# Optimization experiments

Hardware: AMD Instinct MI355X
Metric: run time of the kernel (lower is better)

The kernel has to match this reference:

```python
import jax, jax.numpy as jnp
import numpy as np

B, M, D, H = 2, 2048, 1024, 16
DH = D // H            # 64 head dim
FF = 2624              # GeGLU intermediate size
EPS = 1e-5
ROPE_BASE = 10000.0


def _layernorm(x, g, b):
    mu = jnp.mean(x, axis=-1, keepdims=True)
    var = jnp.mean(jnp.square(x - mu), axis=-1, keepdims=True)
    return (x - mu) * jax.lax.rsqrt(var + EPS) * g + b


def _rope_cos_sin(m, dh):
    # HF-style: inv_freq over even dims; only first dh/2 entries are used by apply_rope
    inv_freq = 1.0 / (ROPE_BASE ** (jnp.arange(0, dh, 2, dtype=jnp.float32) / dh))  # [dh/2]
    ang = jnp.arange(m, dtype=jnp.float32)[:, None] * inv_freq[None, :]             # [M, dh/2]
    return jnp.cos(ang), jnp.sin(ang)


def _apply_rope(x, c, s):
    # x: [B,H,M,dh]; c,s: [M,dh/2] broadcast over B,H. Half-split (non-interleaved) rotation.
    x1, x2 = jnp.split(x, 2, axis=-1)
    return jnp.concatenate([x1 * c - x2 * s, x1 * s + x2 * c], axis=-1)


def setup_inputs() -> dict:
    key = jax.random.key(0)
    ks = jax.random.split(key, 6)
    w = lambda k, shape: (jax.random.normal(k, shape, jnp.float32) * 0.02)
    return {
        "hidden_states": jax.random.normal(ks[0], (B, M, D), jnp.float32),
        "attention_mask": jnp.ones((B, M), jnp.int32),
        "ln1_g": jnp.ones((D,), jnp.float32),
        "ln1_b": jnp.zeros((D,), jnp.float32),
        "Wqkv_w": w(ks[1], (3 * D, D)),
        "Wqkv_b": jnp.zeros((3 * D,), jnp.float32),
        "Wo_w": w(ks[2], (D, D)),
        "ln2_g": jnp.ones((D,), jnp.float32),
        "ln2_b": jnp.zeros((D,), jnp.float32),
        "Wi_w": w(ks[3], (2 * FF, D)),
        "Wmlp_o_w": w(ks[4], (D, FF)),
    }


def reference(hidden_states, attention_mask, ln1_g, ln1_b, Wqkv_w, Wqkv_b, Wo_w,
              ln2_g, ln2_b, Wi_w, Wmlp_o_w):
    x = hidden_states                                    # [B,M,D]
    xn = _layernorm(x, ln1_g, ln1_b)
    qkv = xn @ Wqkv_w.T + Wqkv_b                         # [B,M,3D]
    qkv = qkv.reshape(B, M, 3, H, DH).transpose(0, 3, 1, 2, 4)  # [B,H,M,3,dh]
    q, k, v = qkv[..., 0, :], qkv[..., 1, :], qkv[..., 2, :]    # each [B,H,M,dh]

    c, s = _rope_cos_sin(M, DH)                          # [M, dh/2]
    q = _apply_rope(q, c, s)
    k = _apply_rope(k, c, s)

    scale = 1.0 / np.sqrt(DH)
    scores = jnp.einsum("bhmd,bhnd->bhmn", q, k) * scale  # [B,H,M,M]
    keep = (attention_mask > 0)[:, None, None, :]         # [B,1,1,M] padding mask on keys
    scores = jnp.where(keep, scores, -jnp.inf)
    p = jax.nn.softmax(scores, axis=-1)
    o = jnp.einsum("bhmn,bhnd->bhmd", p, v)               # [B,H,M,dh]

    attn_out = o.transpose(0, 2, 1, 3).reshape(B, M, D)
    x = x + attn_out @ Wo_w.T

    # ModernBERT GeGLU MLP: input, gate = Wi(x).chunk(2); Wo(gelu(input) * gate)
    xn2 = _layernorm(x, ln2_g, ln2_b)
    hg = xn2 @ Wi_w.T                                     # [B,M,2*FF]
    h_in, h_gate = jnp.split(hg, 2, axis=-1)
    x = x + (jax.nn.gelu(h_in) * h_gate) @ Wmlp_o_w.T
    return x
```

## Files before the change

### kernel.cpp

```cpp
#include <hip/hip_runtime.h>
#include <cstdint>
#include <cstddef>

using u16 = unsigned short;
using u32 = uint32_t;

typedef __attribute__((ext_vector_type(8))) short short8;
typedef __attribute__((ext_vector_type(4))) float floatx4;
typedef __attribute__((ext_vector_type(4))) unsigned int uintx4;

#define DEVFN static __device__ __forceinline__

#define QSCALE 0.18033688011112042f

DEVFN u16 f2bf(float f) {
  u32 u = __float_as_uint(f);
  return (u16)((u + 0x7fffu + ((u >> 16) & 1u)) >> 16);
}

DEVFN float b2f(u16 u) { return __uint_as_float(((u32)u) << 16); }

DEVFN u32 pkbf(float lo, float hi) {
  return __builtin_amdgcn_perm(__float_as_uint(hi) + 0x8000u,
                               __float_as_uint(lo) + 0x8000u, 0x07060302u);
}

DEVFN void async_load16(const void* g, const void* lds) {
  __builtin_amdgcn_global_load_lds(
      (const __attribute__((address_space(1))) u32*)(uintptr_t)g,
      (__attribute__((address_space(3))) u32*)(u32)(uintptr_t)lds,
      16, 0, 0);
}

DEVFN void cvt4(const float* __restrict__ src, u16* __restrict__ dst, int i) {
  const float4 v = ((const float4*)src)[i];
  ushort4 o;
  o.x = f2bf(v.x); o.y = f2bf(v.y); o.z = f2bf(v.z); o.w = f2bf(v.w);
  ((ushort4*)dst)[i] = o;
}

__global__ __launch_bounds__(256)
void prep_k(const float* __restrict__ Wqkv, const float* __restrict__ Wo,
            const float* __restrict__ Wi, const float* __restrict__ Wmlp,
            const float* __restrict__ hidden, const float* __restrict__ ln1g,
            const float* __restrict__ ln1b,
            u16* __restrict__ wqkv_bf, u16* __restrict__ wo_bf,
            u16* __restrict__ wi_bf, u16* __restrict__ wmlp_bf,
            float* __restrict__ ct, float* __restrict__ st, u16* __restrict__ xn) {
  const int bid = blockIdx.x;
  const int tid = threadIdx.x;
  __shared__ float red[8];
  if (bid < 256) {
    const int i = bid * 256 + tid;
    const int m = i >> 5, f = i & 31;
    const float inv = exp2f((float)f * -0.41524101186092025f);
    const float ang = (float)m * inv;
    ct[i] = cosf(ang);
    st[i] = sinf(ang);
  } else if (bid < 3328) {
    cvt4(Wqkv, wqkv_bf, (bid - 256) * 256 + tid);
  } else if (bid < 4352) {
    cvt4(Wo, wo_bf, (bid - 3328) * 256 + tid);
  } else if (bid < 9600) {
    const int i = (bid - 4352) * 256 + tid;
    const int i4 = i * 4;
    const int p = i4 >> 10, kc = i4 & 1023;
    const int g = p >> 5, c = p & 31;
    const int srow = (c < 16) ? (g * 16 + c) : (2624 + g * 16 + (c - 16));
    const float4 v = *(const float4*)(Wi + (size_t)srow * 1024 + kc);
    ushort4 o;
    o.x = f2bf(v.x); o.y = f2bf(v.y); o.z = f2bf(v.z); o.w = f2bf(v.w);
    ((ushort4*)wi_bf)[i] = o;
  } else if (bid < 12224) {
    cvt4(Wmlp, wmlp_bf, (bid - 9600) * 256 + tid);
  } else {
    const int row = bid - 12224;
    const float4 v = ((const float4*)(hidden + (size_t)row * 1024))[tid];
    float s = v.x + v.y + v.z + v.w;
    float ss = v.x * v.x + v.y * v.y + v.z * v.z + v.w * v.w;
#pragma unroll
    for (int d = 32; d > 0; d >>= 1) {
      s += __shfl_xor(s, d);
      ss += __shfl_xor(ss, d);
    }
    const int wave = tid >> 6;
    if ((tid & 63) == 0) { red[wave] = s; red[4 + wave] = ss; }
    __syncthreads();
    s = red[0] + red[1] + red[2] + red[3];
    ss = red[4] + red[5] + red[6] + red[7];
    const float mu = s * (1.f / 1024.f);
    const float var = ss * (1.f / 1024.f) - mu * mu;
    const float rr = rsqrtf(var + 1e-5f);
    const float4 gv = ((const float4*)ln1g)[tid];
    const float4 bv = ((const float4*)ln1b)[tid];
    u16* orow = xn + (size_t)row * 1024 + tid * 4;
    orow[0] = f2bf((v.x - mu) * rr * gv.x + bv.x);
    orow[1] = f2bf((v.y - mu) * rr * gv.y + bv.y);
    orow[2] = f2bf((v.z - mu) * rr * gv.z + bv.z);
    orow[3] = f2bf((v.w - mu) * rr * gv.w + bv.w);
  }
}

__global__ __launch_bounds__(256)
void red_ln_k(const float* __restrict__ resid, const u16* __restrict__ p0,
              const u16* __restrict__ p1, const u16* __restrict__ p2,
              const float* __restrict__ g, const float* __restrict__ bb,
              float* __restrict__ outx, u16* __restrict__ outn) {
  const int row = blockIdx.x;
  const int tid = threadIdx.x;
  const size_t base = (size_t)row * 1024;
  const float4 h = ((const float4*)(resid + base))[tid];
  const ushort4 a = ((const ushort4*)(p0 + base))[tid];
  const ushort4 c = ((const ushort4*)(p1 + base))[tid];
  const ushort4 d = ((const ushort4*)(p2 + base))[tid];
  float4 v;
  v.x = h.x + b2f(a.x) + b2f(c.x) + b2f(d.x);
  v.y = h.y + b2f(a.y) + b2f(c.y) + b2f(d.y);
  v.z = h.z + b2f(a.z) + b2f(c.z) + b2f(d.z);
  v.w = h.w + b2f(a.w) + b2f(c.w) + b2f(d.w);
  float s = v.x + v.y + v.z + v.w;
  float ss = v.x * v.x + v.y * v.y + v.z * v.z + v.w * v.w;
#pragma unroll
  for (int dd = 32; dd > 0; dd >>= 1) {
    s += __shfl_xor(s, dd);
    ss += __shfl_xor(ss, dd);
  }
  __shared__ float red[8];
  const int wave = tid >> 6;
  if ((tid & 63) == 0) { red[wave] = s; red[4 + wave] = ss; }
  __syncthreads();
  s = red[0] + red[1] + red[2] + red[3];
  ss = red[4] + red[5] + red[6] + red[7];
  const float mu = s * (1.f / 1024.f);
  const float var = ss * (1.f / 1024.f) - mu * mu;
  const float rr = rsqrtf(var + 1e-5f);
  ((float4*)(outx + base))[tid] = v;
  const float4 gv = ((const float4*)g)[tid];
  const float4 bv = ((const float4*)bb)[tid];
  u16* orow = outn + base + tid * 4;
  orow[0] = f2bf((v.x - mu) * rr * gv.x + bv.x);
  orow[1] = f2bf((v.y - mu) * rr * gv.y + bv.y);
  orow[2] = f2bf((v.z - mu) * rr * gv.z + bv.z);
  orow[3] = f2bf((v.w - mu) * rr * gv.w + bv.w);
}

__global__ void red_add_k(float* __restrict__ out, const u16* __restrict__ p0,
                          const u16* __restrict__ p1, const u16* __restrict__ p2,
                          const u16* __restrict__ p3) {
  const int i = blockIdx.x * 256 + threadIdx.x;
  float4 v = ((const float4*)out)[i];
  const ushort4 a = ((const ushort4*)p0)[i];
  const ushort4 c = ((const ushort4*)p1)[i];
  const ushort4 d = ((const ushort4*)p2)[i];
  const ushort4 e = ((const ushort4*)p3)[i];
  v.x += b2f(a.x) + b2f(c.x) + b2f(d.x) + b2f(e.x);
  v.y += b2f(a.y) + b2f(c.y) + b2f(d.y) + b2f(e.y);
  v.z += b2f(a.z) + b2f(c.z) + b2f(d.z) + b2f(e.z);
  v.w += b2f(a.w) + b2f(c.w) + b2f(d.w) + b2f(e.w);
  ((float4*)out)[i] = v;
}

__global__ __launch_bounds__(256)
void red_att_k(u16* __restrict__ att, const u16* __restrict__ p0,
               const float* __restrict__ li0, const float* __restrict__ li1) {
  const int i = blockIdx.x * 256 + threadIdx.x;
  const int i4 = i * 4;
  const int row = i4 >> 10;
  const int col = i4 & 1023;
  const int b = row >> 11, m = row & 2047;
  const int h = col >> 6;
  const int bhm = (b * 16 + h) * 2048 + m;
  const float rl = 1.f / (li0[bhm] + li1[bhm]);
  const ushort4 a = ((const ushort4*)p0)[i];
  const ushort4 c = ((const ushort4*)att)[i];
  ushort4 o;
  o.x = f2bf((b2f(a.x) + b2f(c.x)) * rl);
  o.y = f2bf((b2f(a.y) + b2f(c.y)) * rl);
  o.z = f2bf((b2f(a.z) + b2f(c.z)) * rl);
  o.w = f2bf((b2f(a.w) + b2f(c.w)) * rl);
  ((ushort4*)att)[i] = o;
}

DEVFN void swizzle_tile(int NT, int& tn, int& tm) {
  const int tpx = gridDim.x >> 3;
  const int p = blockIdx.x;
  const int lid = (p & 7) * tpx + (p >> 3);
  const int band = lid / (8 * NT);
  const int rem = lid - band * 8 * NT;
  tn = (rem >> 3) * 128;
  tm = (band * 8 + (rem & 7)) * 128;
}

struct EpiArgs {
  const float* bias;
  u16* q; u16* kk; u16* vt;
  u16* outbf;
  const float* ct; const float* st;
};

template <int EPI>
__global__ __launch_bounds__(256, 3)
void gemm_k(const u16* __restrict__ A, const u16* __restrict__ B, int K, int NT,
            EpiArgs ea) {
  __shared__ __align__(16) u16 sA[2][4096];
  __shared__ __align__(16) u16 sB[2][4096];
  int tn, tm;
  swizzle_tile(NT, tn, tm);
  const int tid = threadIdx.x;
  const int wave = tid >> 6, lane = tid & 63;
  const int quad = lane >> 4, l15 = lane & 15;
  const int wm = (wave >> 1) * 64, wn = (wave & 1) * 64;

  floatx4 acc[4][4];
#pragma unroll
  for (int i = 0; i < 4; ++i)
#pragma unroll
    for (int j = 0; j < 4; ++j) acc[i][j] = (floatx4){0.f, 0.f, 0.f, 0.f};

  const int srow = lane >> 2;
  const int skc = (lane & 3) * 8;
  const int q0i = wave * 2;
  const int row0 = q0i * 16 + srow;
  const int row1 = row0 + 16;
  const size_t aoff0 = (size_t)(tm + row0) * K + skc;
  const size_t aoff1 = (size_t)(tm + row1) * K + skc;
  const size_t boff0 = (size_t)(tn + row0) * K + skc;
  const size_t boff1 = (size_t)(tn + row1) * K + skc;

  async_load16(A + aoff0, (const char*)sA[0] + q0i * 1024);
  async_load16(B + boff0, (const char*)sB[0] + q0i * 1024);
  async_load16(A + aoff1, (const char*)sA[0] + (q0i + 1) * 1024);
  async_load16(B + boff1, (const char*)sB[0] + (q0i + 1) * 1024);

  int buf = 0;
  for (int k0 = 0; k0 < K; k0 += 32) {
    __syncthreads();
    if (k0 + 32 < K) {
      const int kn = k0 + 32;
      async_load16(A + aoff0 + kn, (const char*)sA[buf ^ 1] + q0i * 1024);
      async_load16(B + boff0 + kn, (const char*)sB[buf ^ 1] + q0i * 1024);
      async_load16(A + aoff1 + kn, (const char*)sA[buf ^ 1] + (q0i + 1) * 1024);
      async_load16(B + boff1 + kn, (const char*)sB[buf ^ 1] + (q0i + 1) * 1024);
    }
    const u16* sAr = sA[buf] + (wm + l15) * 32 + quad * 8;
    const u16* sBr = sB[buf] + (wn + l15) * 32 + quad * 8;
    short8 af[4], bfr[4];
#pragma unroll
    for (int t = 0; t < 4; ++t) af[t] = *(const short8*)(sAr + t * 512);
#pragma unroll
    for (int t = 0; t < 4; ++t) bfr[t] = *(const short8*)(sBr + t * 512);
#pragma unroll
    for (int ti = 0; ti < 4; ++ti)
#pragma unroll
      for (int tj = 0; tj < 4; ++tj)
        acc[ti][tj] = __builtin_amdgcn_mfma_f32_16x16x32_bf16(af[ti], bfr[tj], acc[ti][tj], 0, 0, 0);
    buf ^= 1;
  }

  if constexpr (EPI == 0) {
    const int col0 = tn + wn;
    const int t = col0 >> 10;
    const int h = (col0 & 1023) >> 6;
    if (t == 2) {
#pragma unroll
      for (int ti = 0; ti < 4; ++ti)
#pragma unroll
        for (int r = 0; r < 4; ++r) {
          const int row = tm + wm + ti * 16 + quad * 4 + r;
          const int b = row >> 11, m = row & 2047;
          const int mp = (m & ~31) | ((m & 12) << 1) | ((m & 16) >> 2) | (m & 3);
#pragma unroll
          for (int tj = 0; tj < 4; ++tj) {
            const int dh = tj * 16 + l15;
            const float v = acc[ti][tj][r] + ea.bias[col0 + dh];
            ea.vt[((size_t)((b * 16 + h) * 64 + dh)) * 2048 + mp] = f2bf(v);
          }
        }
    } else {
      u16* dst = (t == 0) ? ea.q : ea.kk;
      const float qs = (t == 0) ? QSCALE : 1.f;
#pragma unroll
      for (int ti = 0; ti < 4; ++ti)
#pragma unroll
        for (int r = 0; r < 4; ++r) {
          const int row = tm + wm + ti * 16 + quad * 4 + r;
          const int b = row >> 11, m = row & 2047;
          u16* drow = dst + ((size_t)(b * 16 + h) * 2048 + m) * 64;
#pragma unroll
          for (int tj = 0; tj < 2; ++tj) {
            const int i = tj * 16 + l15;
            const float x1 = acc[ti][tj][r] + ea.bias[col0 + i];
            const float x2 = acc[ti][tj + 2][r] + ea.bias[col0 + 32 + i];
            const float cs = ea.ct[m * 32 + i];
            const float sn = ea.st[m * 32 + i];
            drow[i] = f2bf((x1 * cs - x2 * sn) * qs);
            drow[32 + i] = f2bf((x1 * sn + x2 * cs) * qs);
          }
        }
    }
  } else {
#pragma unroll
    for (int ti = 0; ti < 4; ++ti)
#pragma unroll
      for (int r = 0; r < 4; ++r) {
        const int row = tm + wm + ti * 16 + quad * 4 + r;
#pragma unroll
        for (int u = 0; u < 2; ++u) {
          const float hin = acc[ti][2 * u][r];
          const float hg = acc[ti][2 * u + 1][r];
          const int a = (((tn + wn) >> 5) + u) * 16 + l15;
          const float t2 = hin + 0.044715f * hin * hin * hin;
          const float e = __builtin_amdgcn_exp2f(t2 * -2.302114768f);
          const float gl = hin * __builtin_amdgcn_rcpf(1.f + e);
          ea.outbf[(size_t)row * 2624 + a] = f2bf(gl * hg);
        }
      }
  }
}

__global__ __launch_bounds__(256, 3)
void gemm_sk4(const u16* __restrict__ A, const u16* __restrict__ B, int K, int NT,
              int kps1, int zsw, int kps2,
              u16* __restrict__ p0, u16* __restrict__ p1,
              u16* __restrict__ p2, u16* __restrict__ p3) {
  __shared__ __align__(16) u16 sA[2][4096];
  __shared__ __align__(16) u16 sB[2][4096];
  int tn, tm;
  swizzle_tile(NT, tn, tm);
  const int z = blockIdx.y;
  int kofs, kps;
  if (z < zsw) { kofs = z * kps1; kps = kps1; }
  else { kofs = zsw * kps1 + (z - zsw) * kps2; kps = kps2; }
  const int tid = threadIdx.x;
  const int wave = tid >> 6, lane = tid & 63;
  const int quad = lane >> 4, l15 = lane & 15;
  const int wm = (wave >> 1) * 64, wn = (wave & 1) * 64;

  floatx4 acc[4][4];
#pragma unroll
  for (int i = 0; i < 4; ++i)
#pragma unroll
    for (int j = 0; j < 4; ++j) acc[i][j] = (floatx4){0.f, 0.f, 0.f, 0.f};

  const int srow = lane >> 2;
  const int skc = (lane & 3) * 8;
  const int q0i = wave * 2;
  const int row0 = q0i * 16 + srow;
  const int row1 = row0 + 16;
  const size_t aoff0 = (size_t)(tm + row0) * K + kofs + skc;
  const size_t aoff1 = (size_t)(tm + row1) * K + kofs + skc;
  const size_t boff0 = (size_t)(tn + row0) * K + kofs + skc;
  const size_t boff1 = (size_t)(tn + row1) * K + kofs + skc;

  async_load16(A + aoff0, (const char*)sA[0] + q0i * 1024);
  async_load16(B + boff0, (const char*)sB[0] + q0i * 1024);
  async_load16(A + aoff1, (const char*)sA[0] + (q0i + 1) * 1024);
  async_load16(B + boff1, (const char*)sB[0] + (q0i + 1) * 1024);

  int buf = 0;
  for (int k0 = 0; k0 < kps; k0 += 32) {
    __syncthreads();
    if (k0 + 32 < kps) {
      const int kn = k0 + 32;
      async_load16(A + aoff0 + kn, (const char*)sA[buf ^ 1] + q0i * 1024);
      async_load16(B + boff0 + kn, (const char*)sB[buf ^ 1] + q0i * 1024);
      async_load16(A + aoff1 + kn, (const char*)sA[buf ^ 1] + (q0i + 1) * 1024);
      async_load16(B + boff1 + kn, (const char*)sB[buf ^ 1] + (q0i + 1) * 1024);
    }
    const u16* sAr = sA[buf] + (wm + l15) * 32 + quad * 8;
    const u16* sBr = sB[buf] + (wn + l15) * 32 + quad * 8;
    short8 af[4], bfr[4];
#pragma unroll
    for (int t = 0; t < 4; ++t) af[t] = *(const short8*)(sAr + t * 512);
#pragma unroll
    for (int t = 0; t < 4; ++t) bfr[t] = *(const short8*)(sBr + t * 512);
#pragma unroll
    for (int ti = 0; ti < 4; ++ti)
#pragma unroll
      for (int tj = 0; tj < 4; ++tj)
        acc[ti][tj] = __builtin_amdgcn_mfma_f32_16x16x32_bf16(af[ti], bfr[tj], acc[ti][tj], 0, 0, 0);
    buf ^= 1;
  }

  u16* part = (z == 0) ? p0 : (z == 1) ? p1 : (z == 2) ? p2 : p3;
#pragma unroll
  for (int ti = 0; ti < 4; ++ti)
#pragma unroll
    for (int r = 0; r < 4; ++r) {
      const int row = tm + wm + ti * 16 + quad * 4 + r;
#pragma unroll
      for (int tj = 0; tj < 4; ++tj)
        part[(size_t)row * 1024 + tn + wn + tj * 16 + l15] = f2bf(acc[ti][tj][r]);
    }
}

DEVFN void attn_stage64(const u16* __restrict__ kg, const u16* __restrict__ vtg,
                        size_t bhk, size_t bhv, int key0, int wave, int lane,
                        const u16* sK, const u16* sV) {
#pragma unroll
  for (int j = 0; j < 4; ++j) {
    const int qi = wave * 4 + j;
    if (qi < 8) {
      async_load16(kg + bhk + (size_t)(key0 + lane) * 64 + qi * 8,
                   (const char*)sK + qi * 1024);
    } else {
      const int vi = qi - 8;
      const int c = vi >> 2, kc = vi & 3;
      async_load16(vtg + bhv + (size_t)lane * 2048 + key0 + c * 32 + kc * 8,
                   (const char*)sV + vi * 1024);
    }
  }
}

__global__ __launch_bounds__(256, 3)
void attn_k(const u16* __restrict__ qg, const u16* __restrict__ kg,
            const u16* __restrict__ vtg, const int* __restrict__ mask,
            u16* __restrict__ p0g, u16* __restrict__ p1g,
            float* __restrict__ li0, float* __restrict__ li1) {
  __shared__ __align__(16) u16 sKV[2][8192];
  const int L = blockIdx.x;
  const int xcd = L & 7, idx = L >> 3;
  const int bh = (xcd << 2) | (idx >> 5);
  const int local = idx & 31;
  const int q0 = (local >> 1) * 128;
  const int z = local & 1;
  const int keyBase = z << 10;
  const int b = bh >> 4, h = bh & 15;
  const int tid = threadIdx.x;
  const int wave = tid >> 6, lane = tid & 63;
  const int quad = lane >> 4, l15 = lane & 15;
  const size_t bhk = (size_t)bh * 2048 * 64;
  const size_t bhv = (size_t)bh * 64 * 2048;

  u32 avbits = 0;
#pragma unroll
  for (int kt = 0; kt < 16; ++kt) {
    const bool ok = mask[b * 2048 + keyBase + kt * 64 + lane] > 0;
    if (__all(ok)) avbits |= (1u << kt);
  }

  short8 aq[2][2];
#pragma unroll
  for (int g = 0; g < 2; ++g) {
    const u16* qptr = qg + ((size_t)bh * 2048 + q0 + wave * 32 + g * 16 + l15) * 64 + quad * 8;
    aq[g][0] = *(const short8*)qptr;
    aq[g][1] = *(const short8*)(qptr + 32);
  }

  floatx4 o[2][4];
#pragma unroll
  for (int g = 0; g < 2; ++g)
#pragma unroll
    for (int t = 0; t < 4; ++t) o[g][t] = (floatx4){0.f, 0.f, 0.f, 0.f};
  float li[2] = {0.f, 0.f};
  const floatx4 z4 = {0.f, 0.f, 0.f, 0.f};

  attn_stage64(kg, vtg, bhk, bhv, keyBase, wave, lane, sKV[0], sKV[0] + 4096);
  __syncthreads();

  int buf = 0;
  for (int kt = 0; kt < 16; ++kt) {
    const u16* sK = sKV[buf];
    const u16* sV = sKV[buf] + 4096;
    const int key0 = keyBase + kt * 64;
    if (kt < 15) {
      attn_stage64(kg, vtg, bhk, bhv, key0 + 64, wave, lane,
                   sKV[buf ^ 1], sKV[buf ^ 1] + 4096);
    }
    const bool allv = (avbits >> kt) & 1u;

    short8 pa[2][2];
#pragma unroll
    for (int g = 0; g < 2; ++g) {
      floatx4 sacc[4];
      __builtin_amdgcn_s_setprio(1);
#pragma unroll
      for (int tj = 0; tj < 4; ++tj) {
        const short8 b0 = *(const short8*)(sK + quad * 512 + (tj * 16 + l15) * 8);
        const short8 b1 = *(const short8*)(sK + (4 + quad) * 512 + (tj * 16 + l15) * 8);
        sacc[tj] = __builtin_amdgcn_mfma_f32_16x16x32_bf16(b0, aq[g][0], z4, 0, 0, 0);
        sacc[tj] = __builtin_amdgcn_mfma_f32_16x16x32_bf16(b1, aq[g][1], sacc[tj], 0, 0, 0);
      }
      __builtin_amdgcn_s_setprio(0);

      if (allv) {
        float sum = li[g];
#pragma unroll
        for (int tj = 0; tj < 4; ++tj)
#pragma unroll
          for (int r = 0; r < 4; ++r) {
            const float p = __builtin_amdgcn_exp2f(sacc[tj][r]);
            sacc[tj][r] = p;
            sum += p;
          }
        li[g] = sum;
      } else {
        float sum = li[g];
#pragma unroll
        for (int tj = 0; tj < 4; ++tj)
#pragma unroll
          for (int r = 0; r < 4; ++r) {
            const int key = key0 + tj * 16 + quad * 4 + r;
            const float mb = (mask[b * 2048 + key] > 0) ? 0.f : -1e30f;
            const float p = __builtin_amdgcn_exp2f(sacc[tj][r] + mb);
            sacc[tj][r] = p;
            sum += p;
          }
        li[g] = sum;
      }

#pragma unroll
      for (int c = 0; c < 2; ++c) {
        uintx4 w;
        w.x = pkbf(sacc[2 * c][0], sacc[2 * c][1]);
        w.y = pkbf(sacc[2 * c][2], sacc[2 * c][3]);
        w.z = pkbf(sacc[2 * c + 1][0], sacc[2 * c + 1][1]);
        w.w = pkbf(sacc[2 * c + 1][2], sacc[2 * c + 1][3]);
        pa[g][c] = __builtin_bit_cast(short8, w);
      }
    }

#pragma unroll
    for (int c = 0; c < 2; ++c) {
      __builtin_amdgcn_s_setprio(1);
#pragma unroll
      for (int tj2 = 0; tj2 < 4; ++tj2) {
        const short8 bv = *(const short8*)(sV + (c * 4 + quad) * 512 + (tj2 * 16 + l15) * 8);
        o[0][tj2] = __builtin_amdgcn_mfma_f32_16x16x32_bf16(pa[0][c], bv, o[0][tj2], 0, 0, 0);
        o[1][tj2] = __builtin_amdgcn_mfma_f32_16x16x32_bf16(pa[1][c], bv, o[1][tj2], 0, 0, 0);
      }
      __builtin_amdgcn_s_setprio(0);
    }
    __syncthreads();
    buf ^= 1;
  }

#pragma unroll
  for (int g = 0; g < 2; ++g) {
    float s = li[g];
    s += __shfl_xor(s, 16);
    s += __shfl_xor(s, 32);
    li[g] = s;
  }

  u16* pz = z ? p1g : p0g;
  float* lz = z ? li1 : li0;
  if (lane < 16) {
#pragma unroll
    for (int g = 0; g < 2; ++g)
      lz[(size_t)bh * 2048 + q0 + wave * 32 + g * 16 + l15] = li[g];
  }

#pragma unroll
  for (int g = 0; g < 2; ++g)
#pragma unroll
    for (int tj = 0; tj < 4; ++tj)
#pragma unroll
      for (int r = 0; r < 4; ++r) {
        const int m = q0 + wave * 32 + g * 16 + quad * 4 + r;
        pz[((size_t)b * 2048 + m) * 1024 + h * 64 + tj * 16 + l15] = f2bf(o[g][tj][r]);
      }
}

static const size_t OFF_WQKV = 0;
static const size_t OFF_WO   = 6291456;
static const size_t OFF_WI   = 8388608;
static const size_t OFF_WMLP = 19136512;
static const size_t OFF_XN   = 24510464;
static const size_t OFF_Q    = 32899072;
static const size_t OFF_K    = 41287680;
static const size_t OFF_VT   = 49676288;
static const size_t OFF_ATT  = 58064896;
static const size_t OFF_ROPE = OFF_ATT;
static const size_t WS_NEED  = 66453504;

extern "C" void kernel_launch(void* const* d_in, const int* in_sizes, int n_in,
                              void* d_out, int out_size, void* d_ws, size_t ws_size,
                              hipStream_t stream) {
  (void)in_sizes; (void)n_in; (void)out_size;
  if (ws_size < WS_NEED) return;

  const float* hidden = (const float*)d_in[0];
  const int*   mask   = (const int*)d_in[1];
  const float* ln1g   = (const float*)d_in[2];
  const float* ln1b   = (const float*)d_in[3];
  const float* Wqkv   = (const float*)d_in[4];
  const float* Wqkvb  = (const float*)d_in[5];
  const float* Wo     = (const float*)d_in[6];
  const float* ln2g   = (const float*)d_in[7];
  const float* ln2b   = (const float*)d_in[8];
  const float* Wi     = (const float*)d_in[9];
  const float* Wmlp   = (const float*)d_in[10];
  float* out = (float*)d_out;
  char* ws = (char*)d_ws;

  u16* wqkv_bf = (u16*)(ws + OFF_WQKV);
  u16* wo_bf   = (u16*)(ws + OFF_WO);
  u16* wi_bf   = (u16*)(ws + OFF_WI);
  u16* wmlp_bf = (u16*)(ws + OFF_WMLP);
  u16* xn      = (u16*)(ws + OFF_XN);
  u16* qb      = (u16*)(ws + OFF_Q);
  u16* kb      = (u16*)(ws + OFF_K);
  u16* vtb     = (u16*)(ws + OFF_VT);
  u16* att     = (u16*)(ws + OFF_ATT);
  u16* act     = (u16*)(ws + OFF_Q);
  float* ct    = (float*)(ws + OFF_ROPE);
  float* st    = (float*)(ws + OFF_ROPE + 262144);
  u16* ap0     = (u16*)(ws + OFF_XN);
  u16* ap1     = (u16*)(ws + OFF_ATT);
  float* li0   = (float*)(ws + OFF_WQKV);
  float* li1   = (float*)(ws + OFF_WQKV + 262144);
  u16* wp0     = (u16*)(ws + OFF_Q);
  u16* wp1     = (u16*)(ws + OFF_K);
  u16* wp2     = (u16*)(ws + OFF_VT);
  u16* mp0     = (u16*)(ws + OFF_XN);
  u16* mp1     = (u16*)(ws + OFF_ATT);
  u16* mp2     = (u16*)(ws + OFF_WI);
  u16* mp3     = (u16*)(ws + OFF_WQKV);

  prep_k<<<16320, 256, 0, stream>>>(Wqkv, Wo, Wi, Wmlp, hidden, ln1g, ln1b,
                                    wqkv_bf, wo_bf, wi_bf, wmlp_bf, ct, st, xn);

  EpiArgs e1 = {Wqkvb, qb, kb, vtb, nullptr, ct, st};
  gemm_k<0><<<768, 256, 0, stream>>>(xn, wqkv_bf, 1024, 24, e1);

  attn_k<<<dim3(1024), 256, 0, stream>>>(qb, kb, vtb, mask, ap0, ap1, li0, li1);
  red_att_k<<<4096, 256, 0, stream>>>(att, ap0, li0, li1);

  gemm_sk4<<<dim3(256, 3), 256, 0, stream>>>(att, wo_bf, 1024, 8, 352, 2, 320,
                                             wp0, wp1, wp2, wp2);
  red_ln_k<<<4096, 256, 0, stream>>>(hidden, wp0, wp1, wp2, ln2g, ln2b, out, xn);

  EpiArgs e3 = {nullptr, nullptr, nullptr, nullptr, act, nullptr, nullptr};
  gemm_k<2><<<1312, 256, 0, stream>>>(xn, wi_bf, 1024, 41, e3);

  gemm_sk4<<<dim3(256, 4), 256, 0, stream>>>(act, wmlp_bf, 2624, 8, 672, 2, 640,
                                             mp0, mp1, mp2, mp3);
  red_add_k<<<4096, 256, 0, stream>>>(out, mp0, mp1, mp2, mp3);
}
```

Measured before the change: 332.1 us.

## Triple-buffer GEMM LDS staging with explicit vmcnt waits and raw barriers

Both GEMM kernels move from double-buffered to triple-buffered LDS tiles, prefetching two K-steps ahead. Each step waits with an explicit s_waitcnt vmcnt(4) and a bare s_barrier instead of __syncthreads, so the next stage's loads can stay in flight. The aim is to hide global-load latency behind the MFMA work. LDS per block grows from 32KB to 48KB, which may limit the 3-blocks-per-CU occupancy target, and correctness now depends on the async loads being counted by vmcnt.

```diff
diff --git a/kernel.cpp b/kernel.cpp
--- a/kernel.cpp
+++ b/kernel.cpp
@@ -198,12 +198,20 @@
   const float* ct; const float* st;
 };
 
+#define GEMM_STAGE(kk, dstA, dstB)                                            \
+  do {                                                                        \
+    async_load16(A + aoff0 + (kk), (const char*)(dstA) + q0i * 1024);         \
+    async_load16(B + boff0 + (kk), (const char*)(dstB) + q0i * 1024);         \
+    async_load16(A + aoff1 + (kk), (const char*)(dstA) + (q0i + 1) * 1024);   \
+    async_load16(B + boff1 + (kk), (const char*)(dstB) + (q0i + 1) * 1024);   \
+  } while (0)
+
 template <int EPI>
 __global__ __launch_bounds__(256, 3)
 void gemm_k(const u16* __restrict__ A, const u16* __restrict__ B, int K, int NT,
             EpiArgs ea) {
-  __shared__ __align__(16) u16 sA[2][4096];
-  __shared__ __align__(16) u16 sB[2][4096];
+  __shared__ __align__(16) u16 sA[3][4096];
+  __shared__ __align__(16) u16 sB[3][4096];
   int tn, tm;
   swizzle_tile(NT, tn, tm);
   const int tid = threadIdx.x;
@@ -226,35 +234,37 @@
   const size_t aoff1 = (size_t)(tm + row1) * K + skc;
   const size_t boff0 = (size_t)(tn + row0) * K + skc;
   const size_t boff1 = (size_t)(tn + row1) * K + skc;
-
-  async_load16(A + aoff0, (const char*)sA[0] + q0i * 1024);
-  async_load16(B + boff0, (const char*)sB[0] + q0i * 1024);
-  async_load16(A + aoff1, (const char*)sA[0] + (q0i + 1) * 1024);
-  async_load16(B + boff1, (const char*)sB[0] + (q0i + 1) * 1024);
-
-  int buf = 0;
-  for (int k0 = 0; k0 < K; k0 += 32) {
-    __syncthreads();
-    if (k0 + 32 < K) {
-      const int kn = k0 + 32;
-      async_load16(A + aoff0 + kn, (const char*)sA[buf ^ 1] + q0i * 1024);
-      async_load16(B + boff0 + kn, (const char*)sB[buf ^ 1] + q0i * 1024);
-      async_load16(A + aoff1 + kn, (const char*)sA[buf ^ 1] + (q0i + 1) * 1024);
-      async_load16(B + boff1 + kn, (const char*)sB[buf ^ 1] + (q0i + 1) * 1024);
-    }
-    const u16* sAr = sA[buf] + (wm + l15) * 32 + quad * 8;
-    const u16* sBr = sB[buf] + (wn + l15) * 32 + quad * 8;
+  const int nsteps = K >> 5;
+
+  GEMM_STAGE(0, sA[0], sB[0]);
+  GEMM_STAGE(32, sA[1], sB[1]);
+
+  int c = 0;
+  for (int t = 0; t < nsteps; ++t) {
+    if (t + 1 < nsteps) {
+      asm volatile("s_waitcnt vmcnt(4)" ::: "memory");
+    } else {
+      asm volatile("s_waitcnt vmcnt(0)" ::: "memory");
+    }
+    __builtin_amdgcn_s_barrier();
+    __builtin_amdgcn_sched_barrier(0);
+    if (t + 2 < nsteps) {
+      const int c2 = (c + 2 >= 3) ? c - 1 : c + 2;
+      GEMM_STAGE((t + 2) * 32, sA[c2], sB[c2]);
+    }
+    const u16* sAr = sA[c] + (wm + l15) * 32 + quad * 8;
+    const u16* sBr = sB[c] + (wn + l15) * 32 + quad * 8;
     short8 af[4], bfr[4];
 #pragma unroll
-    for (int t = 0; t < 4; ++t) af[t] = *(const short8*)(sAr + t * 512);
-#pragma unroll
-    for (int t = 0; t < 4; ++t) bfr[t] = *(const short8*)(sBr + t * 512);
+    for (int t2 = 0; t2 < 4; ++t2) af[t2] = *(const short8*)(sAr + t2 * 512);
+#pragma unroll
+    for (int t2 = 0; t2 < 4; ++t2) bfr[t2] = *(const short8*)(sBr + t2 * 512);
 #pragma unroll
     for (int ti = 0; ti < 4; ++ti)
 #pragma unroll
       for (int tj = 0; tj < 4; ++tj)
         acc[ti][tj] = __builtin_amdgcn_mfma_f32_16x16x32_bf16(af[ti], bfr[tj], acc[ti][tj], 0, 0, 0);
-    buf ^= 1;
+    c = (c == 2) ? 0 : c + 1;
   }
 
   if constexpr (EPI == 0) {
@@ -323,8 +333,8 @@
               int kps1, int zsw, int kps2,
               u16* __restrict__ p0, u16* __restrict__ p1,
               u16* __restrict__ p2, u16* __restrict__ p3) {
-  __shared__ __align__(16) u16 sA[2][4096];
-  __shared__ __align__(16) u16 sB[2][4096];
+  __shared__ __align__(16) u16 sA[3][4096];
+  __shared__ __align__(16) u16 sB[3][4096];
   int tn, tm;
   swizzle_tile(NT, tn, tm);
   const int z = blockIdx.y;
@@ -351,35 +361,37 @@
   const size_t aoff1 = (size_t)(tm + row1) * K + kofs + skc;
   const size_t boff0 = (size_t)(tn + row0) * K + kofs + skc;
   const size_t boff1 = (size_t)(tn + row1) * K + kofs + skc;
-
-  async_load16(A + aoff0, (const char*)sA[0] + q0i * 1024);
-  async_load16(B + boff0, (const char*)sB[0] + q0i * 1024);
-  async_load16(A + aoff1, (const char*)sA[0] + (q0i + 1) * 1024);
-  async_load16(B + boff1, (const char*)sB[0] + (q0i + 1) * 1024);
-
-  int buf = 0;
-  for (int k0 = 0; k0 < kps; k0 += 32) {
-    __syncthreads();
-    if (k0 + 32 < kps) {
-      const int kn = k0 + 32;
-      async_load16(A + aoff0 + kn, (const char*)sA[buf ^ 1] + q0i * 1024);
-      async_load16(B + boff0 + kn, (const char*)sB[buf ^ 1] + q0i * 1024);
-      async_load16(A + aoff1 + kn, (const char*)sA[buf ^ 1] + (q0i + 1) * 1024);
-      async_load16(B + boff1 + kn, (const char*)sB[buf ^ 1] + (q0i + 1) * 1024);
-    }
-    const u16* sAr = sA[buf] + (wm + l15) * 32 + quad * 8;
-    const u16* sBr = sB[buf] + (wn + l15) * 32 + quad * 8;
+  const int nsteps = kps >> 5;
+
+  GEMM_STAGE(0, sA[0], sB[0]);
+  GEMM_STAGE(32, sA[1], sB[1]);
+
+  int c = 0;
+  for (int t = 0; t < nsteps; ++t) {
+    if (t + 1 < nsteps) {
+      asm volatile("s_waitcnt vmcnt(4)" ::: "memory");
+    } else {
+      asm volatile("s_waitcnt vmcnt(0)" ::: "memory");
+    }
+    __builtin_amdgcn_s_barrier();
+    __builtin_amdgcn_sched_barrier(0);
+    if (t + 2 < nsteps) {
+      const int c2 = (c + 2 >= 3) ? c - 1 : c + 2;
+      GEMM_STAGE((t + 2) * 32, sA[c2], sB[c2]);
+    }
+    const u16* sAr = sA[c] + (wm + l15) * 32 + quad * 8;
+    const u16* sBr = sB[c] + (wn + l15) * 32 + quad * 8;
     short8 af[4], bfr[4];
 #pragma unroll
-    for (int t = 0; t < 4; ++t) af[t] = *(const short8*)(sAr + t * 512);
-#pragma unroll
-    for (int t = 0; t < 4; ++t) bfr[t] = *(const short8*)(sBr + t * 512);
+    for (int t2 = 0; t2 < 4; ++t2) af[t2] = *(const short8*)(sAr + t2 * 512);
+#pragma unroll
+    for (int t2 = 0; t2 < 4; ++t2) bfr[t2] = *(const short8*)(sBr + t2 * 512);
 #pragma unroll
     for (int ti = 0; ti < 4; ++ti)
 #pragma unroll
       for (int tj = 0; tj < 4; ++tj)
         acc[ti][tj] = __builtin_amdgcn_mfma_f32_16x16x32_bf16(af[ti], bfr[tj], acc[ti][tj], 0, 0, 0);
-    buf ^= 1;
+    c = (c == 2) ? 0 : c + 1;
   }
 
   u16* part = (z == 0) ? p0 : (z == 1) ? p1 : (z == 2) ? p2 : p3;
```

New measurement: 335.1 us. No clear change (+0.9%).
